# Performance work log

Hardware: AMD Instinct MI355X
Metric: run time of the kernel (lower is better)

Reference implementation:

```python
import jax, jax.numpy as jnp
import numpy as np

N_NODES = 50000
N_EDGES = 600000
N_GRAPHS = 64
D = 128  # node/edge/global feature dim
NUM_CLASSES = 10
NUM_PASSES = 3


def setup_inputs() -> dict:
    key = jax.random.key(0)
    ks = jax.random.split(key, 12)
    node_attr = jax.random.normal(ks[0], (N_NODES, D), jnp.float32)
    edge_attr = jax.random.normal(ks[1], (N_EDGES, D), jnp.float32)
    u = jax.random.normal(ks[2], (N_GRAPHS, D), jnp.float32)
    edge_index = jax.random.randint(ks[3], (2, N_EDGES), 0, N_NODES, jnp.int64 if jax.config.jax_enable_x64 else jnp.int32)
    batch = jnp.sort(jax.random.randint(ks[4], (N_NODES,), 0, N_GRAPHS, jnp.int32))
    s = 1.0 / np.sqrt(D)
    We_w = jax.random.normal(ks[5], (4 * D, D), jnp.float32) * s
    We_b = jnp.zeros((D,), jnp.float32)
    Wn_w = jax.random.normal(ks[6], (3 * D, D), jnp.float32) * s
    Wn_b = jnp.zeros((D,), jnp.float32)
    Wg_w = jax.random.normal(ks[7], (3 * D, D), jnp.float32) * s
    Wg_b = jnp.zeros((D,), jnp.float32)
    lin_w = jax.random.normal(ks[8], (3 * D, NUM_CLASSES), jnp.float32) * s
    lin_b = jnp.zeros((NUM_CLASSES,), jnp.float32)
    return {"node_attr": node_attr, "edge_attr": edge_attr, "u": u,
            "edge_index": edge_index, "batch": batch,
            "We_w": We_w, "We_b": We_b, "Wn_w": Wn_w, "Wn_b": Wn_b,
            "Wg_w": Wg_w, "Wg_b": Wg_b, "lin_w": lin_w, "lin_b": lin_b}


def _segment_mean(x, seg, num_segments):
    s = jax.ops.segment_sum(x, seg, num_segments=num_segments)
    cnt = jax.ops.segment_sum(jnp.ones((x.shape[0],), x.dtype), seg, num_segments=num_segments)
    return s / jnp.maximum(cnt, 1.0)[:, None]


def reference(node_attr, edge_attr, u, edge_index, batch,
              We_w, We_b, Wn_w, Wn_b, Wg_w, Wg_b, lin_w, lin_b):
    src = edge_index[0]
    dst = edge_index[1]
    n_nodes = node_attr.shape[0]
    n_graphs = u.shape[0]
    edge_bar = None
    for _ in range(NUM_PASSES):
        # edge update: phi_e([h_src, h_dst, e, u[batch_src]])
        e_in = jnp.concatenate(
            [node_attr[src], node_attr[dst], edge_attr, u[batch[src]]], axis=1)
        edge_attr = jax.nn.relu(e_in @ We_w + We_b)
        # node update: mean of incoming edges per dest node, then phi_n
        edge_bar = _segment_mean(edge_attr, dst, n_nodes)  # [N, D]
        n_in = jnp.concatenate([node_attr, edge_bar, u[batch]], axis=1)
        node_attr = jax.nn.relu(n_in @ Wn_w + Wn_b)
        # global update: per-graph means, then phi_g
        node_mean = _segment_mean(node_attr, batch, n_graphs)
        eb_mean = _segment_mean(edge_bar, batch, n_graphs)
        g_in = jnp.concatenate([node_mean, eb_mean, u], axis=1)
        u = jax.nn.relu(g_in @ Wg_w + Wg_b)
    # readout: concat + global mean pool + linear classifier
    graph_attr = jnp.concatenate([node_attr, edge_bar, u[batch]], axis=1)  # [N, 3D]
    pooled = _segment_mean(graph_attr, batch, n_graphs)  # [G, 3D]
    return pooled @ lin_w + lin_b
```

## Files before the change

kernel.cpp:

```cpp
#include <hip/hip_runtime.h>
#include <math.h>

#define D 128

typedef short bf16x8 __attribute__((ext_vector_type(8)));
typedef float f32x4 __attribute__((ext_vector_type(4)));

__device__ __forceinline__ ushort f2b(float f) {
    union { float f; unsigned u; } v; v.f = f;
    unsigned r = v.u + 0x7FFFu + ((v.u >> 16) & 1u);
    return (ushort)(r >> 16);
}
__device__ __forceinline__ float b2f(ushort b) {
    union { unsigned u; float f; } v; v.u = ((unsigned)b) << 16;
    return v.f;
}
__device__ __forceinline__ void gl_lds16(const void* g, void* l) {
    __builtin_amdgcn_global_load_lds(
        (const __attribute__((address_space(1))) void*)g,
        (__attribute__((address_space(3))) void*)l, 16, 0, 0);
}
__device__ __forceinline__ int lower_bound_i(const int* __restrict__ a, int n, int v) {
    int lo = 0, hi = n;
    while (lo < hi) { int m = (lo + hi) >> 1; if (a[m] < v) lo = m + 1; else hi = m; }
    return lo;
}

__global__ void count_kernel(const int* __restrict__ dst, int* __restrict__ cnt, int E) {
    int e = blockIdx.x * blockDim.x + threadIdx.x;
    if (e < E) atomicAdd(&cnt[dst[e]], 1);
}

__global__ void scan_kernel(const int* __restrict__ cnt, int* __restrict__ offs, int N) {
    __shared__ int part[1024];
    const int t = threadIdx.x;
    const int chunk = (N + 1023) >> 10;
    int lo = t * chunk; if (lo > N) lo = N;
    int hi = lo + chunk; if (hi > N) hi = N;
    int s = 0;
    for (int i = lo; i < hi; ++i) s += cnt[i];
    part[t] = s;
    __syncthreads();
    if (t == 0) {
        int a = 0;
        for (int i = 0; i < 1024; ++i) { int v = part[i]; part[i] = a; a += v; }
        offs[N] = a;
    }
    __syncthreads();
    int a = part[t];
    for (int i = lo; i < hi; ++i) { offs[i] = a; a += cnt[i]; }
}

__global__ void scatter_kernel(const int* __restrict__ dst, const int* __restrict__ offs,
                               int* __restrict__ fill, int* __restrict__ csr, int E) {
    int e = blockIdx.x * blockDim.x + threadIdx.x;
    if (e < E) {
        int d = dst[e];
        int p = offs[d] + atomicAdd(&fill[d], 1);
        csr[p] = e;
    }
}

__global__ void prep_kernel(
    float* __restrict__ edge,
    const float* __restrict__ node, ushort* __restrict__ node_bf,
    const float* __restrict__ u, ushort* __restrict__ u_bf,
    const float* __restrict__ We_w, ushort* __restrict__ Wet,
    const float* __restrict__ Wn_w, ushort* __restrict__ Wnt,
    int N, int G, int E)
{
    const int gid = blockIdx.x * 256 + threadIdx.x;
    const int c0 = E * 32;
    const int c1 = c0 + N * D / 4;
    const int c2 = c1 + G * D / 4;
    const int c3 = c2 + 512 * D;
    const int c4 = c3 + 384 * D;
    if (gid < c0) {
        int row = gid >> 5, q = gid & 31;
        float4 v = *(const float4*)(edge + (size_t)row * D + q * 4);
        ushort4 o; o.x = f2b(v.x); o.y = f2b(v.y); o.z = f2b(v.z); o.w = f2b(v.w);
        *(ushort4*)((ushort*)edge + (size_t)row * 256 + q * 4) = o;
    } else if (gid < c1) {
        int i = (gid - c0) * 4;
        float4 v = *(const float4*)(node + i);
        ushort4 o; o.x = f2b(v.x); o.y = f2b(v.y); o.z = f2b(v.z); o.w = f2b(v.w);
        *(ushort4*)(node_bf + i) = o;
    } else if (gid < c2) {
        int i = (gid - c1) * 4;
        float4 v = *(const float4*)(u + i);
        ushort4 o; o.x = f2b(v.x); o.y = f2b(v.y); o.z = f2b(v.z); o.w = f2b(v.w);
        *(ushort4*)(u_bf + i) = o;
    } else if (gid < c3) {
        int i = gid - c2;
        int k = i >> 7, n = i & 127;
        Wet[(size_t)n * 512 + k] = f2b(We_w[i]);
    } else if (gid < c4) {
        int i = gid - c3;
        int k = i >> 7, n = i & 127;
        Wnt[(size_t)n * 384 + k] = f2b(Wn_w[i]);
    }
}

__global__ __launch_bounds__(256, 2) void edge_gemm(
    const ushort* __restrict__ node_bf, ushort* __restrict__ edge_u,
    const ushort* __restrict__ u_bf,
    const int* __restrict__ src, const int* __restrict__ dst,
    const int* __restrict__ batch,
    const ushort* __restrict__ Wt, const float* __restrict__ bias, int E)
{
    __shared__ ushort As[256 * 32];
    __shared__ ushort Bs[128 * 32];
    __shared__ int rs[256], rd[256], rb[256];

    const int tid = threadIdx.x;
    const int w = tid >> 6, l = tid & 63;
    const int e0 = blockIdx.x * 256;

    {
        int e = e0 + tid; if (e >= E) e = E - 1;
        int s = src[e];
        rs[tid] = s; rd[tid] = dst[e]; rb[tid] = batch[s];
    }

    f32x4 acc[4][8];
#pragma unroll
    for (int i = 0; i < 4; ++i)
#pragma unroll
        for (int j = 0; j < 8; ++j) acc[i][j] = (f32x4)0.0f;

    const int wm = w * 64;
    float bj8[8];
#pragma unroll
    for (int j = 0; j < 8; ++j) bj8[j] = bias[j * 16 + (l & 15)];

    const int srow = l >> 2;
    const int part = (l & 3) * 8;

    __syncthreads();

    for (int c = 0; c < 16; ++c) {
        const int srcsel = c >> 2;
        const int kl = (c & 3) * 32;

#pragma unroll
        for (int t = 0; t < 4; ++t) {
            const int s = w * 4 + t;
            const int row = s * 16 + srow;
            const ushort* gp;
            if (srcsel == 0)      gp = node_bf + (size_t)rs[row] * D + kl + part;
            else if (srcsel == 1) gp = node_bf + (size_t)rd[row] * D + kl + part;
            else if (srcsel == 2) { int e = e0 + row; if (e >= E) e = E - 1;
                                    gp = edge_u + (size_t)e * 256 + kl + part; }
            else                  gp = u_bf + (size_t)rb[row] * D + kl + part;
            gl_lds16(gp, &As[s * 512]);
        }
#pragma unroll
        for (int t = 0; t < 2; ++t) {
            const int s = w + t * 4;
            const int n = s * 16 + srow;
            gl_lds16(Wt + (size_t)n * 512 + c * 32 + part, &Bs[s * 512]);
        }
        __syncthreads();

        bf16x8 af[4], bfr[8];
#pragma unroll
        for (int i = 0; i < 4; ++i)
            af[i] = *(const bf16x8*)&As[(wm + i * 16 + (l & 15)) * 32 + (l >> 4) * 8];
#pragma unroll
        for (int j = 0; j < 8; ++j)
            bfr[j] = *(const bf16x8*)&Bs[(j * 16 + (l & 15)) * 32 + (l >> 4) * 8];
#pragma unroll
        for (int i = 0; i < 4; ++i)
#pragma unroll
            for (int j = 0; j < 8; ++j)
                acc[i][j] = __builtin_amdgcn_mfma_f32_16x16x32_bf16(af[i], bfr[j], acc[i][j], 0, 0, 0);
        __syncthreads();
    }

#pragma unroll
    for (int i = 0; i < 4; ++i) {
#pragma unroll
        for (int r = 0; r < 4; ++r) {
            const int m = wm + i * 16 + (l >> 4) * 4 + r;
            const int e = e0 + m;
            if (e < E) {
                ushort* ep = edge_u + (size_t)e * 256;
#pragma unroll
                for (int j = 0; j < 8; ++j) {
                    float v = fmaxf(acc[i][j][r] + bj8[j], 0.0f);
                    ep[j * 16 + (l & 15)] = f2b(v);
                }
            }
        }
    }
}

__global__ void gather_ebar(const ushort* __restrict__ edge_u, const int* __restrict__ offs,
                            const int* __restrict__ csr, ushort* __restrict__ ebar_bf, int N)
{
    int n = blockIdx.x * 8 + (threadIdx.x >> 5);
    int q = threadIdx.x & 31;
    if (n >= N) return;
    int lo = offs[n], hi = offs[n + 1];
    float s0 = 0.0f, s1 = 0.0f, s2 = 0.0f, s3 = 0.0f;
    for (int j = lo; j < hi; ++j) {
        int e = csr[j];
        ushort4 v = *(const ushort4*)(edge_u + (size_t)e * 256 + q * 4);
        s0 += b2f(v.x); s1 += b2f(v.y); s2 += b2f(v.z); s3 += b2f(v.w);
    }
    float inv = 1.0f / (float)max(hi - lo, 1);
    ushort4 o; o.x = f2b(s0 * inv); o.y = f2b(s1 * inv); o.z = f2b(s2 * inv); o.w = f2b(s3 * inv);
    *(ushort4*)(ebar_bf + (size_t)n * D + q * 4) = o;
}

__global__ __launch_bounds__(256) void node_gemm(
    ushort* __restrict__ node_bf, const ushort* __restrict__ ebar_bf,
    const ushort* __restrict__ u_bf, const int* __restrict__ batch,
    const ushort* __restrict__ Wt, const float* __restrict__ bias, int N)
{
    __shared__ ushort As[128 * 32];
    __shared__ ushort Bs[128 * 32];
    __shared__ int rb[128];

    const int tid = threadIdx.x;
    const int w = tid >> 6, l = tid & 63;
    const int n0 = blockIdx.x * 128;

    if (tid < 128) {
        int n = n0 + tid; if (n >= N) n = N - 1;
        rb[tid] = batch[n];
    }

    f32x4 acc[4][4];
#pragma unroll
    for (int i = 0; i < 4; ++i)
#pragma unroll
        for (int j = 0; j < 4; ++j) acc[i][j] = (f32x4)0.0f;

    const int wm = (w >> 1) * 64, wn = (w & 1) * 64;
    float bj4[4];
#pragma unroll
    for (int j = 0; j < 4; ++j) bj4[j] = bias[wn + j * 16 + (l & 15)];

    const int srow = l >> 2;
    const int part = (l & 3) * 8;

    __syncthreads();

    for (int c = 0; c < 12; ++c) {
        const int srcsel = c >> 2;
        const int kl = (c & 3) * 32;

#pragma unroll
        for (int t = 0; t < 2; ++t) {
            const int s = w + t * 4;
            const int row = s * 16 + srow;
            int n = n0 + row; if (n >= N) n = N - 1;
            const ushort* gp;
            if (srcsel == 0)      gp = node_bf + (size_t)n * D + kl + part;
            else if (srcsel == 1) gp = ebar_bf + (size_t)n * D + kl + part;
            else                  gp = u_bf + (size_t)rb[row] * D + kl + part;
            gl_lds16(gp, &As[s * 512]);
        }
#pragma unroll
        for (int t = 0; t < 2; ++t) {
            const int s = w + t * 4;
            const int n = s * 16 + srow;
            gl_lds16(Wt + (size_t)n * 384 + c * 32 + part, &Bs[s * 512]);
        }
        __syncthreads();

        bf16x8 af[4], bfr[4];
#pragma unroll
        for (int i = 0; i < 4; ++i)
            af[i] = *(const bf16x8*)&As[(wm + i * 16 + (l & 15)) * 32 + (l >> 4) * 8];
#pragma unroll
        for (int j = 0; j < 4; ++j)
            bfr[j] = *(const bf16x8*)&Bs[(wn + j * 16 + (l & 15)) * 32 + (l >> 4) * 8];
#pragma unroll
        for (int i = 0; i < 4; ++i)
#pragma unroll
            for (int j = 0; j < 4; ++j)
                acc[i][j] = __builtin_amdgcn_mfma_f32_16x16x32_bf16(af[i], bfr[j], acc[i][j], 0, 0, 0);
        __syncthreads();
    }

#pragma unroll
    for (int i = 0; i < 4; ++i) {
#pragma unroll
        for (int r = 0; r < 4; ++r) {
            const int m = wm + i * 16 + (l >> 4) * 4 + r;
            const int n = n0 + m;
            if (n < N) {
#pragma unroll
                for (int j = 0; j < 4; ++j) {
                    float v = fmaxf(acc[i][j][r] + bj4[j], 0.0f);
                    node_bf[(size_t)n * D + wn + j * 16 + (l & 15)] = f2b(v);
                }
            }
        }
    }
}

__global__ void reduce_partial(
    const ushort* __restrict__ node_bf, const ushort* __restrict__ ebar_bf,
    const int* __restrict__ batch,
    float* __restrict__ nsum, float* __restrict__ esum, int N)
{
    const int col = threadIdx.x & 127;
    const int half = threadIdx.x >> 7;
    const int r0 = blockIdx.x * 128;
    float sn = 0.0f, se = 0.0f;
    int cur = -1;
    for (int ri = half; ri < 128; ri += 2) {
        int r = r0 + ri;
        if (r >= N) break;
        int g = batch[r];
        if (g != cur) {
            if (cur >= 0) {
                atomicAdd(&nsum[cur * D + col], sn);
                atomicAdd(&esum[cur * D + col], se);
            }
            cur = g; sn = 0.0f; se = 0.0f;
        }
        sn += b2f(node_bf[(size_t)r * D + col]);
        se += b2f(ebar_bf[(size_t)r * D + col]);
    }
    if (cur >= 0) {
        atomicAdd(&nsum[cur * D + col], sn);
        atomicAdd(&esum[cur * D + col], se);
    }
}

__global__ void finalize_global(
    float* __restrict__ nsum, float* __restrict__ esum,
    const int* __restrict__ batch,
    float* __restrict__ nmean, float* __restrict__ emean,
    float* __restrict__ u, ushort* __restrict__ u_bf,
    const float* __restrict__ W, const float* __restrict__ bias, int N)
{
    __shared__ float gin[384];
    __shared__ int cnt_s;
    const int g = blockIdx.x;
    const int j = threadIdx.x;
    if (j == 0) {
        int lo = lower_bound_i(batch, N, g);
        int hi = lower_bound_i(batch, N, g + 1);
        cnt_s = hi - lo;
    }
    __syncthreads();
    float inv = 1.0f / (float)max(cnt_s, 1);
    float nm = nsum[g * D + j] * inv;
    float em = esum[g * D + j] * inv;
    nmean[g * D + j] = nm;
    emean[g * D + j] = em;
    nsum[g * D + j] = 0.0f;
    esum[g * D + j] = 0.0f;
    gin[j] = nm; gin[128 + j] = em; gin[256 + j] = u[g * D + j];
    __syncthreads();
    float s = bias[j];
    for (int k = 0; k < 384; ++k) s += gin[k] * W[(size_t)k * D + j];
    float v = fmaxf(s, 0.0f);
    u[g * D + j] = v;
    u_bf[g * D + j] = f2b(v);
}

__global__ void out_kernel(
    const float* __restrict__ nmean, const float* __restrict__ emean,
    const float* __restrict__ u, const int* __restrict__ batch,
    const float* __restrict__ lw, const float* __restrict__ lb,
    float* __restrict__ out, int N, int NC)
{
    __shared__ float pin[384];
    __shared__ int cntg;
    const int g = blockIdx.x;
    const int t = threadIdx.x;
    if (t == 0) {
        int lo = lower_bound_i(batch, N, g);
        int hi = lower_bound_i(batch, N, g + 1);
        cntg = hi - lo;
    }
    __syncthreads();
    if (t < 128)       pin[t] = nmean[g * D + t];
    else if (t < 256)  pin[t] = emean[g * D + (t - 128)];
    else               pin[t] = (cntg > 0) ? u[g * D + (t - 256)] : 0.0f;
    __syncthreads();
    int c = t >> 5, wv = t & 31;
    if (c < NC) {
        float s = 0.0f;
        for (int k = wv; k < 384; k += 32) s += pin[k] * lw[(size_t)k * NC + c];
#pragma unroll
        for (int off = 16; off > 0; off >>= 1) s += __shfl_down(s, off, 32);
        if (wv == 0) out[g * NC + c] = s + lb[c];
    }
}

extern "C" void kernel_launch(void* const* d_in, const int* in_sizes, int n_in,
                              void* d_out, int out_size, void* d_ws, size_t ws_size,
                              hipStream_t stream) {
    float* node = (float*)d_in[0];
    float* edge = (float*)d_in[1];
    float* u    = (float*)d_in[2];
    const int* eidx  = (const int*)d_in[3];
    const int* batch = (const int*)d_in[4];
    const float* We_w = (const float*)d_in[5];
    const float* We_b = (const float*)d_in[6];
    const float* Wn_w = (const float*)d_in[7];
    const float* Wn_b = (const float*)d_in[8];
    const float* Wg_w = (const float*)d_in[9];
    const float* Wg_b = (const float*)d_in[10];
    const float* lin_w = (const float*)d_in[11];
    const float* lin_b = (const float*)d_in[12];

    const int N = in_sizes[0] / D;
    const int E = in_sizes[3] / 2;
    const int G = in_sizes[2] / D;
    const int NC = out_size / G;
    const int* src = eidx;
    const int* dst = eidx + E;

    char* p = (char*)d_ws;
    auto carve = [&](size_t bytes) { void* r = p; p += (bytes + 255) & ~(size_t)255; return r; };
    int*    cnt     = (int*)carve((size_t)N * 4);
    int*    fill    = (int*)carve((size_t)N * 4);
    float*  nsum    = (float*)carve((size_t)G * D * 4);
    float*  esum    = (float*)carve((size_t)G * D * 4);
    size_t  zspan   = (size_t)(p - (char*)cnt);
    int*    offs    = (int*)carve((size_t)(N + 1) * 4);
    int*    csr     = (int*)carve((size_t)E * 4);
    ushort* node_bf = (ushort*)carve((size_t)N * D * 2);
    ushort* ebar_bf = (ushort*)carve((size_t)N * D * 2);
    ushort* u_bf    = (ushort*)carve((size_t)G * D * 2);
    ushort* Wet     = (ushort*)carve((size_t)512 * D * 2);
    ushort* Wnt     = (ushort*)carve((size_t)384 * D * 2);
    float*  nmean   = (float*)carve((size_t)G * D * 4);
    float*  emean   = (float*)carve((size_t)G * D * 4);

    ushort* edge_u = (ushort*)edge;

    hipMemsetAsync(cnt, 0, zspan, stream);

    count_kernel<<<(E + 255) / 256, 256, 0, stream>>>(dst, cnt, E);
    scan_kernel<<<1, 1024, 0, stream>>>(cnt, offs, N);
    scatter_kernel<<<(E + 255) / 256, 256, 0, stream>>>(dst, offs, fill, csr, E);

    const int prep_units = E * 32 + N * D / 4 + G * D / 4 + 512 * D + 384 * D;
    prep_kernel<<<(prep_units + 255) / 256, 256, 0, stream>>>(
        edge, node, node_bf, u, u_bf, We_w, Wet, Wn_w, Wnt, N, G, E);

    const int edge_blocks = (E + 255) / 256;
    const int node_blocks = (N + 127) / 128;
    const int red_blocks  = (N + 127) / 128;

    for (int pass = 0; pass < 3; ++pass) {
        edge_gemm<<<edge_blocks, 256, 0, stream>>>(node_bf, edge_u, u_bf, src, dst, batch,
                                                   Wet, We_b, E);
        gather_ebar<<<(N + 7) / 8, 256, 0, stream>>>(edge_u, offs, csr, ebar_bf, N);
        node_gemm<<<node_blocks, 256, 0, stream>>>(node_bf, ebar_bf, u_bf, batch,
                                                   Wnt, Wn_b, N);
        reduce_partial<<<red_blocks, 256, 0, stream>>>(node_bf, ebar_bf, batch, nsum, esum, N);
        finalize_global<<<G, 128, 0, stream>>>(nsum, esum, batch, nmean, emean,
                                               u, u_bf, Wg_w, Wg_b, N);
    }
    out_kernel<<<G, 384, 0, stream>>>(nmean, emean, u, batch, lin_w, lin_b,
                                      (float*)d_out, N, NC);
}
```

Measured before the change: 1.247 ms.

## Factor edge GEMM into per-node and per-graph projections gathered in epilogue

Splits the concatenated edge MLP weight: node_src and node_dst blocks are projected once per node (N×256 fp32 via a new MFMA kernel), the u block plus bias once per graph, and the per-edge GEMM now only multiplies the edge features (K=128 instead of 512). The epilogue gathers the src/dst/u projections and adds them before ReLU. This cuts edge GEMM FLOPs by about 4x and removes the gathered A-tile loads, at the cost of two extra launches per pass, a 51 MB fp32 intermediate, and random fp32 gathers in the epilogue. It also keeps the node and u contributions in fp32 rather than rounding their inputs to bf16, which changes the numerics slightly.

After: 1.331 ms. 1.07x slower.

```diff
diff --git a/kernel.cpp b/kernel.cpp
--- a/kernel.cpp
+++ b/kernel.cpp
@@ -65,7 +65,7 @@
     float* __restrict__ edge,
     const float* __restrict__ node, ushort* __restrict__ node_bf,
     const float* __restrict__ u, ushort* __restrict__ u_bf,
-    const float* __restrict__ We_w, ushort* __restrict__ Wet,
+    const float* __restrict__ We_w, ushort* __restrict__ Bt12, ushort* __restrict__ W3t,
     const float* __restrict__ Wn_w, ushort* __restrict__ Wnt,
     int N, int G, int E)
 {
@@ -93,7 +93,13 @@
     } else if (gid < c3) {
         int i = gid - c2;
         int k = i >> 7, n = i & 127;
-        Wet[(size_t)n * 512 + k] = f2b(We_w[i]);
+        if (k < 384) {
+            ushort b = f2b(We_w[i]);
+            if (k < 256)
+                Bt12[(((size_t)((k >> 7) << 7) + n) << 7) + (k & 127)] = b;
+            else
+                W3t[((size_t)n << 7) + (k - 256)] = b;
+        }
     } else if (gid < c4) {
         int i = gid - c3;
         int k = i >> 7, n = i & 127;
@@ -101,12 +107,92 @@
     }
 }
 
+__global__ void uproj_kernel(const float* __restrict__ u, const float* __restrict__ We_w,
+                             const float* __restrict__ We_b, float* __restrict__ upf)
+{
+    __shared__ float us[128];
+    const int g = blockIdx.x;
+    const int j = threadIdx.x;
+    us[j] = u[g * D + j];
+    __syncthreads();
+    float s = We_b[j];
+    for (int k = 0; k < 128; ++k) s += us[k] * We_w[(size_t)(384 + k) * D + j];
+    upf[g * D + j] = s;
+}
+
+__global__ __launch_bounds__(256) void nproj_gemm(
+    const ushort* __restrict__ node_bf, const ushort* __restrict__ Bt12,
+    float* __restrict__ npf, int N)
+{
+    __shared__ ushort As[128 * 32];
+    __shared__ ushort Bs[256 * 32];
+
+    const int tid = threadIdx.x;
+    const int w = tid >> 6, l = tid & 63;
+    const int n0 = blockIdx.x * 128;
+
+    f32x4 acc[4][8];
+#pragma unroll
+    for (int i = 0; i < 4; ++i)
+#pragma unroll
+        for (int j = 0; j < 8; ++j) acc[i][j] = (f32x4)0.0f;
+
+    const int wm = (w >> 1) * 64, wn = (w & 1) * 128;
+    const int srow = l >> 2;
+    const int part = (l & 3) * 8;
+
+    for (int c = 0; c < 4; ++c) {
+        const int kl = c * 32;
+#pragma unroll
+        for (int t = 0; t < 2; ++t) {
+            const int s = w + t * 4;
+            int n = n0 + s * 16 + srow; if (n >= N) n = N - 1;
+            gl_lds16(node_bf + (size_t)n * D + kl + part, &As[s * 512]);
+        }
+#pragma unroll
+        for (int t = 0; t < 4; ++t) {
+            const int s = w * 4 + t;
+            const int n = s * 16 + srow;
+            gl_lds16(Bt12 + (size_t)n * 128 + kl + part, &Bs[s * 512]);
+        }
+        __syncthreads();
+
+        bf16x8 af[4], bfr[8];
+#pragma unroll
+        for (int i = 0; i < 4; ++i)
+            af[i] = *(const bf16x8*)&As[(wm + i * 16 + (l & 15)) * 32 + (l >> 4) * 8];
+#pragma unroll
+        for (int j = 0; j < 8; ++j)
+            bfr[j] = *(const bf16x8*)&Bs[(wn + j * 16 + (l & 15)) * 32 + (l >> 4) * 8];
+#pragma unroll
+        for (int i = 0; i < 4; ++i)
+#pragma unroll
+            for (int j = 0; j < 8; ++j)
+                acc[i][j] = __builtin_amdgcn_mfma_f32_16x16x32_bf16(af[i], bfr[j], acc[i][j], 0, 0, 0);
+        __syncthreads();
+    }
+
+#pragma unroll
+    for (int i = 0; i < 4; ++i) {
+#pragma unroll
+        for (int r = 0; r < 4; ++r) {
+            const int m = wm + i * 16 + (l >> 4) * 4 + r;
+            const int n = n0 + m;
+            if (n < N) {
+#pragma unroll
+                for (int j = 0; j < 8; ++j)
+                    npf[(size_t)n * 256 + wn + j * 16 + (l & 15)] = acc[i][j][r];
+            }
+        }
+    }
+}
+
 __global__ __launch_bounds__(256, 2) void edge_gemm(
-    const ushort* __restrict__ node_bf, ushort* __restrict__ edge_u,
-    const ushort* __restrict__ u_bf,
+    ushort* __restrict__ edge_u,
+    const float* __restrict__ npf, const float* __restrict__ upf,
     const int* __restrict__ src, const int* __restrict__ dst,
     const int* __restrict__ batch,
-    const ushort* __restrict__ Wt, const float* __restrict__ bias, int E)
+    const ushort* __restrict__ W3t, int E)
 {
     __shared__ ushort As[256 * 32];
     __shared__ ushort Bs[128 * 32];
@@ -129,36 +215,25 @@
         for (int j = 0; j < 8; ++j) acc[i][j] = (f32x4)0.0f;
 
     const int wm = w * 64;
-    float bj8[8];
-#pragma unroll
-    for (int j = 0; j < 8; ++j) bj8[j] = bias[j * 16 + (l & 15)];
-
     const int srow = l >> 2;
     const int part = (l & 3) * 8;
 
     __syncthreads();
 
-    for (int c = 0; c < 16; ++c) {
-        const int srcsel = c >> 2;
-        const int kl = (c & 3) * 32;
+    for (int c = 0; c < 4; ++c) {
+        const int kl = c * 32;
 
 #pragma unroll
         for (int t = 0; t < 4; ++t) {
             const int s = w * 4 + t;
-            const int row = s * 16 + srow;
-            const ushort* gp;
-            if (srcsel == 0)      gp = node_bf + (size_t)rs[row] * D + kl + part;
-            else if (srcsel == 1) gp = node_bf + (size_t)rd[row] * D + kl + part;
-            else if (srcsel == 2) { int e = e0 + row; if (e >= E) e = E - 1;
-                                    gp = edge_u + (size_t)e * 256 + kl + part; }
-            else                  gp = u_bf + (size_t)rb[row] * D + kl + part;
-            gl_lds16(gp, &As[s * 512]);
+            int e = e0 + s * 16 + srow; if (e >= E) e = E - 1;
+            gl_lds16(edge_u + (size_t)e * 256 + kl + part, &As[s * 512]);
         }
 #pragma unroll
         for (int t = 0; t < 2; ++t) {
             const int s = w + t * 4;
             const int n = s * 16 + srow;
-            gl_lds16(Wt + (size_t)n * 512 + c * 32 + part, &Bs[s * 512]);
+            gl_lds16(W3t + (size_t)n * 128 + kl + part, &Bs[s * 512]);
         }
         __syncthreads();
 
@@ -177,6 +252,7 @@
         __syncthreads();
     }
 
+    const int cc = l & 15;
 #pragma unroll
     for (int i = 0; i < 4; ++i) {
 #pragma unroll
@@ -184,11 +260,15 @@
             const int m = wm + i * 16 + (l >> 4) * 4 + r;
             const int e = e0 + m;
             if (e < E) {
+                const float* p1 = npf + (size_t)rs[m] * 256;
+                const float* p2 = npf + (size_t)rd[m] * 256 + 128;
+                const float* pu = upf + (size_t)rb[m] * D;
                 ushort* ep = edge_u + (size_t)e * 256;
 #pragma unroll
                 for (int j = 0; j < 8; ++j) {
-                    float v = fmaxf(acc[i][j][r] + bj8[j], 0.0f);
-                    ep[j * 16 + (l & 15)] = f2b(v);
+                    const int col = j * 16 + cc;
+                    float v = acc[i][j][r] + p1[col] + p2[col] + pu[col];
+                    ep[col] = f2b(fmaxf(v, 0.0f));
                 }
             }
         }
@@ -431,10 +511,13 @@
     ushort* node_bf = (ushort*)carve((size_t)N * D * 2);
     ushort* ebar_bf = (ushort*)carve((size_t)N * D * 2);
     ushort* u_bf    = (ushort*)carve((size_t)G * D * 2);
-    ushort* Wet     = (ushort*)carve((size_t)512 * D * 2);
+    ushort* Bt12    = (ushort*)carve((size_t)256 * 128 * 2);
+    ushort* W3t     = (ushort*)carve((size_t)128 * 128 * 2);
     ushort* Wnt     = (ushort*)carve((size_t)384 * D * 2);
     float*  nmean   = (float*)carve((size_t)G * D * 4);
     float*  emean   = (float*)carve((size_t)G * D * 4);
+    float*  upf     = (float*)carve((size_t)G * D * 4);
+    float*  npf     = (float*)carve((size_t)N * 256 * 4);
 
     ushort* edge_u = (ushort*)edge;
 
@@ -446,15 +529,18 @@
 
     const int prep_units = E * 32 + N * D / 4 + G * D / 4 + 512 * D + 384 * D;
     prep_kernel<<<(prep_units + 255) / 256, 256, 0, stream>>>(
-        edge, node, node_bf, u, u_bf, We_w, Wet, Wn_w, Wnt, N, G, E);
+        edge, node, node_bf, u, u_bf, We_w, Bt12, W3t, Wn_w, Wnt, N, G, E);
 
     const int edge_blocks = (E + 255) / 256;
     const int node_blocks = (N + 127) / 128;
+    const int proj_blocks = (N + 127) / 128;
     const int red_blocks  = (N + 127) / 128;
 
     for (int pass = 0; pass < 3; ++pass) {
-        edge_gemm<<<edge_blocks, 256, 0, stream>>>(node_bf, edge_u, u_bf, src, dst, batch,
-                                                   Wet, We_b, E);
+        uproj_kernel<<<G, 128, 0, stream>>>(u, We_w, We_b, upf);
+        nproj_gemm<<<proj_blocks, 256, 0, stream>>>(node_bf, Bt12, npf, N);
+        edge_gemm<<<edge_blocks, 256, 0, stream>>>(edge_u, npf, upf, src, dst, batch,
+                                                   W3t, E);
         gather_ebar<<<(N + 7) / 8, 256, 0, stream>>>(edge_u, offs, csr, ebar_bf, N);
         node_gemm<<<node_blocks, 256, 0, stream>>>(node_bf, ebar_bf, u_bf, batch,
                                                    Wnt, Wn_b, N);
```
